# Optimization experiments

Hardware: AMD Instinct MI355X
Metric: run time of the kernel (lower is better)

The kernel has to match this reference:

```python
import math
import jax, jax.numpy as jnp
import numpy as np

DRAGON_ITERATIONS = 12
DRAGON_SMOOTHING = 0.1


def _dragon_patterns(iterations=DRAGON_ITERATIONS, smoothing=DRAGON_SMOOTHING):
    """Deterministic (non-learned) Dragon curve patterns, matching torch impl."""
    patterns = [np.array([0.5], dtype=np.float32)]
    kernel = np.ones(3, dtype=np.float32) / 3.0
    for _ in range(1, iterations):
        prev = patterns[-1]
        n = len(prev)
        newp = np.zeros(2 * n + 1, dtype=np.float32)
        newp[:n] = prev
        newp[n] = 0.5
        newp[n + 1:] = 1.0 - prev[::-1]
        if smoothing > 0:
            # conv1d with kernel_size=3, padding=1 (zero pad) == np.convolve 'same'
            newp = np.convolve(newp, kernel, mode='same').astype(np.float32)
        newp = (newp - newp.min()) / (newp.max() - newp.min() + 1e-8)
        patterns.append(newp.astype(np.float32))
    return patterns

_PATTERNS = _dragon_patterns()


def _interp_pattern(seq_len):
    """Linearly interpolate selected dragon pattern to seq_len (static shapes)."""
    it = min(int(math.log2(seq_len)), DRAGON_ITERATIONS - 1)
    pattern = _PATTERNS[it]
    if len(pattern) == seq_len:
        w = pattern.copy()
    else:
        x_old = np.linspace(0.0, 1.0, len(pattern), dtype=np.float64)
        x_new = np.linspace(0.0, 1.0, seq_len, dtype=np.float64)
        w = np.interp(x_new, x_old, pattern.astype(np.float64)).astype(np.float32)
    return it, jnp.asarray(w)


def setup_inputs() -> dict:
    key = jax.random.key(0)
    ks = jax.random.split(key, 8)
    B, S, D = 8, 2048, 512
    query = jax.random.normal(ks[0], (B, S, D), dtype=jnp.float32)
    k = jax.random.normal(ks[1], (B, S, D), dtype=jnp.float32)
    value = jax.random.normal(ks[2], (B, S, D), dtype=jnp.float32)
    pattern_scale = jnp.ones((DRAGON_ITERATIONS,), dtype=jnp.float32)
    pattern_bias = jnp.zeros((DRAGON_ITERATIONS,), dtype=jnp.float32)
    w1 = jax.random.normal(ks[3], (DRAGON_ITERATIONS, 64), dtype=jnp.float32) * (1.0 / math.sqrt(DRAGON_ITERATIONS))
    b1 = jnp.zeros((64,), dtype=jnp.float32)
    w2 = jax.random.normal(ks[4], (64, 1), dtype=jnp.float32) * (1.0 / 8.0)
    b2 = jnp.zeros((1,), dtype=jnp.float32)
    return {"query": query, "key": k, "value": value,
            "pattern_scale": pattern_scale, "pattern_bias": pattern_bias,
            "w1": w1, "b1": b1, "w2": w2, "b2": b2}


def reference(query, key, value, pattern_scale, pattern_bias, w1, b1, w2, b2):
    B, S, D = key.shape
    it, base_w = _interp_pattern(S)
    # learned affine + softplus on dragon weights
    dragon_w = jax.nn.softplus(base_w * pattern_scale[it] + pattern_bias[it])  # [S]
    weighted_keys = key * dragon_w[None, :, None]                              # [B,S,D]
    scores = jnp.einsum('bqd,bkd->bqk', query, weighted_keys) / math.sqrt(D)   # [B,S,S]
    attn = jax.nn.softmax(scores, axis=-1)
    # blend factor from one-hot iteration features through tiny MLP
    feat = jax.nn.one_hot(it, DRAGON_ITERATIONS, dtype=query.dtype)            # [12]
    h = jax.nn.relu(feat @ w1 + b1)
    blend = jax.nn.sigmoid(h @ w2 + b2)                                        # [1]
    blend = blend[0]
    final_attn = blend * attn + (1.0 - blend) / S                              # uniform blend
    out = jnp.einsum('bqk,bkd->bqd', final_attn, value)                        # [B,S,D]
    # original does output.squeeze(1); S>1 so it's a no-op here
    return out
```

## Files before the change

kernel.cpp:

```cpp
#include <hip/hip_runtime.h>
#include <cstdint>

#define DEV __device__ __forceinline__

typedef float f32x4 __attribute__((ext_vector_type(4)));
typedef short s16x8 __attribute__((ext_vector_type(8)));

DEV unsigned short f2bf(float f){
    unsigned u = __builtin_bit_cast(unsigned, f);
    u = u + 0x7fffu + ((u >> 16) & 1u);
    return (unsigned short)(u >> 16);
}
DEV float bf2f(unsigned short h){
    unsigned u = ((unsigned)h) << 16;
    return __builtin_bit_cast(float, u);
}

typedef const void __attribute__((address_space(1)))* gcp;
typedef void __attribute__((address_space(3)))* lp;
DEV void gload_lds16(const void* g, void* l){
    __builtin_amdgcn_global_load_lds((gcp)g, (lp)l, 16, 0, 0);
}

DEV void bar(){ asm volatile("s_barrier" ::: "memory"); }
#define WAIT_VM(n) asm volatile("s_waitcnt vmcnt(" #n ")" ::: "memory")
#define LDSFENCE   asm volatile("s_waitcnt lgkmcnt(0)" ::: "memory")

__global__ __launch_bounds__(256) void k_stage1(
    const float* __restrict__ Q, const float* __restrict__ K,
    const float* __restrict__ V,
    const float* __restrict__ scale, const float* __restrict__ bias,
    const float* __restrict__ w1, const float* __restrict__ b1,
    const float* __restrict__ w2, const float* __restrict__ b2,
    float* __restrict__ dragon_w, float* __restrict__ blend_out,
    unsigned short* __restrict__ Qb, unsigned short* __restrict__ Kb,
    unsigned short* __restrict__ Vt, float* __restrict__ vmean_part)
{
    __shared__ float sh[8704];
    int tid = threadIdx.x;
    int bx  = blockIdx.x;

    if (bx == 0){
        float* A  = sh;
        float* Bb = sh + 4096;
        if (tid < 64){
            if (tid == 0) A[0] = 0.5f;
            LDSFENCE;
            int len = 1;
            const float third = 1.0f/3.0f;
            for (int it = 1; it < 12; ++it){
                int n = len, nl = 2*n + 1;
                for (int i = tid; i < nl; i += 64){
                    float v;
                    if (i < n)       v = A[i];
                    else if (i == n) v = 0.5f;
                    else             v = 1.0f - A[2*n - i];
                    Bb[i] = v;
                }
                LDSFENCE;
                float mn = 3.4e38f, mx = -3.4e38f;
                for (int i = tid; i < nl; i += 64){
                    float s = Bb[i]*third;
                    if (i > 0)    s += Bb[i-1]*third;
                    if (i < nl-1) s += Bb[i+1]*third;
                    A[i] = s;
                    mn = fminf(mn, s); mx = fmaxf(mx, s);
                }
                #pragma unroll
                for (int off = 32; off > 0; off >>= 1){
                    mn = fminf(mn, __shfl_xor(mn, off, 64));
                    mx = fmaxf(mx, __shfl_xor(mx, off, 64));
                }
                float lo = mn, den = mx - lo + 1e-8f;
                for (int i = tid; i < nl; i += 64) A[i] = (A[i] - lo) / den;
                LDSFENCE;
                len = nl;
            }
        }
        __syncthreads();
        float sc = scale[11], bi = bias[11];
        for (int i = tid; i < 2048; i += 256){
            float x = A[2*i]*sc + bi;
            dragon_w[i] = fmaxf(x, 0.f) + log1pf(__expf(-fabsf(x)));
        }
        if (tid < 64){
            float h = fmaxf(w1[11*64 + tid] + b1[tid], 0.f);
            float c = h * w2[tid];
            for (int off = 32; off > 0; off >>= 1) c += __shfl_xor(c, off, 64);
            if (tid == 0) blend_out[0] = 1.f/(1.f + __expf(-(c + b2[0])));
        }
        return;
    }

    if (bx <= 4096){
        const float* src = (bx <= 2048) ? Q : K;
        unsigned short* dst = (bx <= 2048) ? Qb : Kb;
        int bi = (bx <= 2048) ? (bx-1) : (bx-2049);
        const long long total4 = (long long)8*2048*512/4;
        long long stride = 2048LL*256;
        for (long long i = (long long)bi*256 + tid; i < total4; i += stride){
            long long base = i*4;
            const float4 q = *(const float4*)(src + base);
            ushort4 qo;
            qo.x = f2bf(q.x); qo.y = f2bf(q.y); qo.z = f2bf(q.z); qo.w = f2bf(q.w);
            *(ushort4*)(dst + base) = qo;
        }
        return;
    }

    int t = bx - 4097;
    int stile = t & 31, dtile = (t >> 5) & 7, b = t >> 8;
    int s0 = stile*64, d0 = dtile*64;
    float (*tile)[67] = (float(*)[67])sh;
    float* red = sh + 4288;
    int c4 = tid & 15, rr = tid >> 4;
    const float* src = V + ((long long)b*2048 + s0)*512 + d0;
    #pragma unroll
    for (int p = 0; p < 4; ++p){
        int row = p*16 + rr;
        const float4 v = *(const float4*)(src + (long long)row*512 + c4*4);
        tile[row][c4*4+0] = v.x; tile[row][c4*4+1] = v.y;
        tile[row][c4*4+2] = v.z; tile[row][c4*4+3] = v.w;
    }
    __syncthreads();
    unsigned short* dst = Vt + ((long long)b*512 + d0)*2048 + s0;
    #pragma unroll
    for (int p = 0; p < 4; ++p){
        int d = p*16 + rr;
        ushort4 o;
        o.x = f2bf(tile[c4*4+0][d]);
        o.y = f2bf(tile[c4*4+1][d]);
        o.z = f2bf(tile[c4*4+2][d]);
        o.w = f2bf(tile[c4*4+3][d]);
        *(ushort4*)(dst + (long long)d*2048 + c4*4) = o;
    }
    int dcol = tid & 63, sp = tid >> 6;
    float s = 0.f;
    #pragma unroll
    for (int ii = 0; ii < 16; ++ii) s += tile[sp*16 + ii][dcol];
    red[sp*64 + dcol] = s;
    __syncthreads();
    if (sp == 0){
        float tot = red[dcol] + red[64+dcol] + red[128+dcol] + red[192+dcol];
        vmean_part[stile*4096 + b*512 + d0 + dcol] = tot * (1.0f/2048.0f);
    }
}

#define SCALE_QK 0.04419417382415922f

__global__ __launch_bounds__(256) void k_gemm_qk(
    const unsigned short* __restrict__ Qb, const unsigned short* __restrict__ Kb,
    const float* __restrict__ dragon_w,
    unsigned short* __restrict__ Sp, float* __restrict__ lpart)
{
    __shared__ unsigned short A0[128*64], B0[128*64];
    __shared__ unsigned short A1[128*64], B1[128*64];
    int tid = threadIdx.x;
    int lane = tid & 63, wave = tid >> 6;
    int wm = wave >> 1, wn = wave & 1;
    int ln = lane & 15, q4 = lane >> 4;
    int sx = ln & 7;
    int lid = (blockIdx.x & 7)*256 + (blockIdx.x >> 3);
    int kb = lid & 15, qb = (lid >> 4) & 15, b = lid >> 8;
    int q0 = qb*128, k0 = kb*128;
    const unsigned short* Abase = Qb + ((long long)b*2048 + q0)*512;
    const unsigned short* Bbase = Kb + ((long long)b*2048 + k0)*512;

    f32x4 acc[4][4];
    #pragma unroll
    for (int i = 0; i < 4; ++i)
        #pragma unroll
        for (int j = 0; j < 4; ++j) acc[i][j] = (f32x4)0.0f;

    int cc = lane & 7;
    int rg = lane >> 3;

    auto STAGE = [&](unsigned short* dA, unsigned short* dB, int kt){
        #pragma unroll
        for (int c = 0; c < 4; ++c){
            int chunk = wave*4 + c;
            int row = chunk*8 + rg;
            int gc  = cc ^ (row & 7);
            gload_lds16(Abase + (long long)row*512 + kt*64 + gc*8, dA + chunk*512);
            gload_lds16(Bbase + (long long)row*512 + kt*64 + gc*8, dB + chunk*512);
        }
    };
    auto COMPUTE = [&](const unsigned short* At, const unsigned short* Bt){
        #pragma unroll
        for (int ks = 0; ks < 2; ++ks){
            s16x8 af[4], bfr[4];
            int cs = ((ks*4 + q4) ^ sx) * 8;
            #pragma unroll
            for (int i = 0; i < 4; ++i)
                af[i] = *(const s16x8*)&At[(wm*64 + i*16 + ln)*64 + cs];
            #pragma unroll
            for (int j = 0; j < 4; ++j)
                bfr[j] = *(const s16x8*)&Bt[(wn*64 + j*16 + ln)*64 + cs];
            __builtin_amdgcn_s_setprio(1);
            #pragma unroll
            for (int i = 0; i < 4; ++i)
                #pragma unroll
                for (int j = 0; j < 4; ++j)
                    acc[i][j] = __builtin_amdgcn_mfma_f32_16x16x32_bf16(af[i], bfr[j], acc[i][j], 0, 0, 0);
            __builtin_amdgcn_s_setprio(0);
        }
    };

    STAGE(A0, B0, 0);
    STAGE(A1, B1, 1);
    WAIT_VM(8); bar();
    #pragma unroll
    for (int t = 0; t < 8; ++t){
        if (t & 1) COMPUTE(A1, B1); else COMPUTE(A0, B0);
        bar();
        int tn = (t + 2) & 7;
        if (t & 1) STAGE(A1, B1, tn); else STAGE(A0, B0, tn);
        WAIT_VM(8);
        bar();
    }
    WAIT_VM(0); bar();

    float wj[4];
    #pragma unroll
    for (int j = 0; j < 4; ++j)
        wj[j] = dragon_w[k0 + wn*64 + j*16 + ln] * SCALE_QK;

    float* lred = (float*)A0;
    unsigned short* outp = Sp + (long long)b*2048*2048;
    #pragma unroll
    for (int i = 0; i < 4; ++i){
        float rs[4] = {0.f, 0.f, 0.f, 0.f};
        #pragma unroll
        for (int j = 0; j < 4; ++j){
            #pragma unroll
            for (int r = 0; r < 4; ++r){
                int q = q0 + wm*64 + i*16 + q4*4 + r;
                int k = k0 + wn*64 + j*16 + ln;
                float v = __expf(acc[i][j][r] * wj[j]);
                unsigned short h = f2bf(v);
                outp[(long long)q*2048 + k] = h;
                rs[r] += bf2f(h);
            }
        }
        #pragma unroll
        for (int r = 0; r < 4; ++r){
            float v = rs[r];
            v += __shfl_xor(v, 1, 16);
            v += __shfl_xor(v, 2, 16);
            v += __shfl_xor(v, 4, 16);
            v += __shfl_xor(v, 8, 16);
            if (ln == 0) lred[(wm*64 + i*16 + q4*4 + r)*2 + wn] = v;
        }
    }
    __syncthreads();
    if (tid < 128)
        lpart[((long long)b*16 + kb)*2048 + q0 + tid] = lred[tid*2] + lred[tid*2+1];
}

__global__ __launch_bounds__(256) void k_gemm_pv(
    const unsigned short* __restrict__ Sp, const unsigned short* __restrict__ Vt,
    const float* __restrict__ lpart, const float* __restrict__ vmean_part,
    const float* __restrict__ blendp, float* __restrict__ out)
{
    __shared__ unsigned short A0[128*64], B0[128*64];
    __shared__ unsigned short A1[128*64], B1[128*64];
    int tid = threadIdx.x;
    int lane = tid & 63, wave = tid >> 6;
    int wm = wave >> 1, wn = wave & 1;
    int ln = lane & 15, q4 = lane >> 4;
    int sx = ln & 7;
    int lid = (blockIdx.x & 7)*64 + (blockIdx.x >> 3);
    int db = lid & 3, qb = (lid >> 2) & 15, b = lid >> 6;
    int q0 = qb*128, d0 = db*128;
    const unsigned short* Abase = Sp + (long long)b*2048*2048 + (long long)q0*2048;
    const unsigned short* Bbase = Vt + ((long long)b*512 + d0)*2048;

    f32x4 acc[4][4];
    #pragma unroll
    for (int i = 0; i < 4; ++i)
        #pragma unroll
        for (int j = 0; j < 4; ++j) acc[i][j] = (f32x4)0.0f;

    int cc = lane & 7;
    int rg = lane >> 3;

    auto STAGE = [&](unsigned short* dA, unsigned short* dB, int kt){
        #pragma unroll
        for (int c = 0; c < 4; ++c){
            int chunk = wave*4 + c;
            int row = chunk*8 + rg;
            int gc  = cc ^ (row & 7);
            gload_lds16(Abase + (long long)row*2048 + kt*64 + gc*8, dA + chunk*512);
            gload_lds16(Bbase + (long long)row*2048 + kt*64 + gc*8, dB + chunk*512);
        }
    };
    auto COMPUTE = [&](const unsigned short* At, const unsigned short* Bt){
        #pragma unroll
        for (int ks = 0; ks < 2; ++ks){
            s16x8 af[4], bfr[4];
            int cs = ((ks*4 + q4) ^ sx) * 8;
            #pragma unroll
            for (int i = 0; i < 4; ++i)
                af[i] = *(const s16x8*)&At[(wm*64 + i*16 + ln)*64 + cs];
            #pragma unroll
            for (int j = 0; j < 4; ++j)
                bfr[j] = *(const s16x8*)&Bt[(wn*64 + j*16 + ln)*64 + cs];
            __builtin_amdgcn_s_setprio(1);
            #pragma unroll
            for (int i = 0; i < 4; ++i)
                #pragma unroll
                for (int j = 0; j < 4; ++j)
                    acc[i][j] = __builtin_amdgcn_mfma_f32_16x16x32_bf16(af[i], bfr[j], acc[i][j], 0, 0, 0);
            __builtin_amdgcn_s_setprio(0);
        }
    };

    STAGE(A0, B0, 0);
    STAGE(A1, B1, 1);
    WAIT_VM(8); bar();
    for (int t = 0; t < 32; ++t){
        if (t & 1) COMPUTE(A1, B1); else COMPUTE(A0, B0);
        bar();
        int tn = (t + 2) & 31;
        if (t & 1) STAGE(A1, B1, tn); else STAGE(A0, B0, tn);
        WAIT_VM(8);
        bar();
    }
    WAIT_VM(0); bar();

    float* l_sh  = (float*)A0;
    float* vm_sh = (float*)B0;
    if (tid < 128){
        float s = 0.f;
        #pragma unroll
        for (int kb = 0; kb < 16; ++kb)
            s += lpart[((long long)b*16 + kb)*2048 + q0 + tid];
        l_sh[tid] = 1.0f / s;
    } else {
        int d = tid - 128;
        float s = 0.f;
        #pragma unroll
        for (int st = 0; st < 32; ++st)
            s += vmean_part[st*4096 + b*512 + d0 + d];
        vm_sh[d] = s;
    }
    __syncthreads();

    float blend = blendp[0];
    float ib = 1.0f - blend;
    float* obase = out + ((long long)b*2048 + q0)*512 + d0;
    float vm[4];
    #pragma unroll
    for (int j = 0; j < 4; ++j) vm[j] = vm_sh[wn*64 + j*16 + ln];
    #pragma unroll
    for (int i = 0; i < 4; ++i){
        #pragma unroll
        for (int r = 0; r < 4; ++r){
            int ql = wm*64 + i*16 + q4*4 + r;
            float linv = l_sh[ql];
            #pragma unroll
            for (int j = 0; j < 4; ++j){
                int dl = wn*64 + j*16 + ln;
                obase[(long long)ql*512 + dl] = blend*acc[i][j][r]*linv + ib*vm[j];
            }
        }
    }
}

extern "C" void kernel_launch(void* const* d_in, const int* in_sizes, int n_in,
                              void* d_out, int out_size, void* d_ws, size_t ws_size,
                              hipStream_t stream)
{
    (void)in_sizes; (void)n_in; (void)out_size; (void)ws_size;
    const float* Q  = (const float*)d_in[0];
    const float* K  = (const float*)d_in[1];
    const float* V  = (const float*)d_in[2];
    const float* ps = (const float*)d_in[3];
    const float* pb = (const float*)d_in[4];
    const float* w1 = (const float*)d_in[5];
    const float* b1 = (const float*)d_in[6];
    const float* w2 = (const float*)d_in[7];
    const float* b2 = (const float*)d_in[8];
    float* out = (float*)d_out;

    char* ws = (char*)d_ws;
    float* dragon_w        = (float*)(ws);
    float* blend           = (float*)(ws + 8192);
    float* vmean_part      = (float*)(ws + 32768);
    size_t off = 32768 + (size_t)512*1024;
    unsigned short* Qb     = (unsigned short*)(ws + off);
    unsigned short* Kb     = (unsigned short*)(ws + off + (size_t)16*1024*1024);
    unsigned short* Vt     = (unsigned short*)(ws + off + (size_t)32*1024*1024);
    unsigned short* Sp     = (unsigned short*)(ws + off + (size_t)48*1024*1024);
    float* lpart           = (float*)(ws + off + (size_t)112*1024*1024);

    hipLaunchKernelGGL(k_stage1,  dim3(6145), dim3(256), 0, stream,
                       Q, K, V, ps, pb, w1, b1, w2, b2, dragon_w, blend,
                       Qb, Kb, Vt, vmean_part);
    hipLaunchKernelGGL(k_gemm_qk, dim3(2048), dim3(256), 0, stream,
                       Qb, Kb, dragon_w, Sp, lpart);
    hipLaunchKernelGGL(k_gemm_pv, dim3(512),  dim3(256), 0, stream,
                       Sp, Vt, lpart, vmean_part, blend, out);
}
```

Measured before the change: 243.6 us.

## Restructure PV GEMM into 256x128 tiles with triple-buffered half-step pipeline

The PV GEMM now uses 512-thread blocks covering 256 query rows by 128 head dims, with LDS buffers tripled and split into halves. Global-to-LDS loads for step t+2 are interleaved with MFMA work on the current step, with barriers and priority hints at each half. The QK kernel's main loop is rewritten as an unrolled stage/compute sequence using __syncthreads and without setprio. The aim is more operand reuse per block and better overlap of memory latency with MFMA work, at the cost of more LDS, fewer blocks and a more delicate synchronisation scheme.

```diff
diff --git a/kernel.cpp b/kernel.cpp
--- a/kernel.cpp
+++ b/kernel.cpp
@@ -196,29 +196,23 @@
             #pragma unroll
             for (int j = 0; j < 4; ++j)
                 bfr[j] = *(const s16x8*)&Bt[(wn*64 + j*16 + ln)*64 + cs];
-            __builtin_amdgcn_s_setprio(1);
             #pragma unroll
             for (int i = 0; i < 4; ++i)
                 #pragma unroll
                 for (int j = 0; j < 4; ++j)
                     acc[i][j] = __builtin_amdgcn_mfma_f32_16x16x32_bf16(af[i], bfr[j], acc[i][j], 0, 0, 0);
-            __builtin_amdgcn_s_setprio(0);
-        }
-    };
-
-    STAGE(A0, B0, 0);
-    STAGE(A1, B1, 1);
-    WAIT_VM(8); bar();
-    #pragma unroll
-    for (int t = 0; t < 8; ++t){
-        if (t & 1) COMPUTE(A1, B1); else COMPUTE(A0, B0);
-        bar();
-        int tn = (t + 2) & 7;
-        if (t & 1) STAGE(A1, B1, tn); else STAGE(A0, B0, tn);
-        WAIT_VM(8);
-        bar();
-    }
-    WAIT_VM(0); bar();
+        }
+    };
+
+    STAGE(A0, B0, 0); __syncthreads();
+    STAGE(A1, B1, 1); COMPUTE(A0, B0); __syncthreads();
+    STAGE(A0, B0, 2); COMPUTE(A1, B1); __syncthreads();
+    STAGE(A1, B1, 3); COMPUTE(A0, B0); __syncthreads();
+    STAGE(A0, B0, 4); COMPUTE(A1, B1); __syncthreads();
+    STAGE(A1, B1, 5); COMPUTE(A0, B0); __syncthreads();
+    STAGE(A0, B0, 6); COMPUTE(A1, B1); __syncthreads();
+    STAGE(A1, B1, 7); COMPUTE(A0, B0); __syncthreads();
+    COMPUTE(A1, B1); __syncthreads();
 
     float wj[4];
     #pragma unroll
@@ -257,23 +251,23 @@
         lpart[((long long)b*16 + kb)*2048 + q0 + tid] = lred[tid*2] + lred[tid*2+1];
 }
 
-__global__ __launch_bounds__(256) void k_gemm_pv(
+__global__ __launch_bounds__(512) void k_gemm_pv(
     const unsigned short* __restrict__ Sp, const unsigned short* __restrict__ Vt,
     const float* __restrict__ lpart, const float* __restrict__ vmean_part,
     const float* __restrict__ blendp, float* __restrict__ out)
 {
-    __shared__ unsigned short A0[128*64], B0[128*64];
-    __shared__ unsigned short A1[128*64], B1[128*64];
+    __shared__ unsigned short At[3][2][128*64];
+    __shared__ unsigned short Bt[3][2][64*64];
     int tid = threadIdx.x;
     int lane = tid & 63, wave = tid >> 6;
-    int wm = wave >> 1, wn = wave & 1;
+    int wm = wave & 3, wn = wave >> 2;
     int ln = lane & 15, q4 = lane >> 4;
-    int sx = ln & 7;
-    int lid = (blockIdx.x & 7)*64 + (blockIdx.x >> 3);
-    int db = lid & 3, qb = (lid >> 2) & 15, b = lid >> 6;
-    int q0 = qb*128, d0 = db*128;
-    const unsigned short* Abase = Sp + (long long)b*2048*2048 + (long long)q0*2048;
-    const unsigned short* Bbase = Vt + ((long long)b*512 + d0)*2048;
+    int cc = lane & 7, rg = lane >> 3;
+    int lid = (blockIdx.x & 7)*32 + (blockIdx.x >> 3);
+    int db = lid & 3, qb = (lid >> 2) & 7, b = lid >> 5;
+    int q0 = qb*256, d0 = db*128;
+    const unsigned short* Ab = Sp + (long long)b*2048*2048 + (long long)q0*2048;
+    const unsigned short* Bb = Vt + ((long long)b*512 + d0)*2048;
 
     f32x4 acc[4][4];
     #pragma unroll
@@ -281,63 +275,82 @@
         #pragma unroll
         for (int j = 0; j < 4; ++j) acc[i][j] = (f32x4)0.0f;
 
-    int cc = lane & 7;
-    int rg = lane >> 3;
-
-    auto STAGE = [&](unsigned short* dA, unsigned short* dB, int kt){
-        #pragma unroll
-        for (int c = 0; c < 4; ++c){
-            int chunk = wave*4 + c;
-            int row = chunk*8 + rg;
-            int gc  = cc ^ (row & 7);
-            gload_lds16(Abase + (long long)row*2048 + kt*64 + gc*8, dA + chunk*512);
-            gload_lds16(Bbase + (long long)row*2048 + kt*64 + gc*8, dB + chunk*512);
-        }
-    };
-    auto COMPUTE = [&](const unsigned short* At, const unsigned short* Bt){
-        #pragma unroll
-        for (int ks = 0; ks < 2; ++ks){
-            s16x8 af[4], bfr[4];
-            int cs = ((ks*4 + q4) ^ sx) * 8;
-            #pragma unroll
-            for (int i = 0; i < 4; ++i)
-                af[i] = *(const s16x8*)&At[(wm*64 + i*16 + ln)*64 + cs];
+    auto STAGE_A = [&](int ts, int h){
+        unsigned short* d = &At[ts % 3][h][0];
+        int tsrc = ts & 31;
+        #pragma unroll
+        for (int c2 = 0; c2 < 2; ++c2){
+            int c = wave*2 + c2;
+            int row = c*8 + rg;
+            gload_lds16(Ab + (long long)(h*128 + row)*2048 + tsrc*64 + (cc^rg)*8,
+                        d + c*512);
+        }
+    };
+    auto STAGE_B = [&](int ts, int g){
+        unsigned short* d = &Bt[ts % 3][g][0];
+        int tsrc = ts & 31;
+        int row = wave*8 + rg;
+        gload_lds16(Bb + (long long)(g*64 + row)*2048 + tsrc*64 + (cc^rg)*8,
+                    d + wave*512);
+    };
+    auto LDA = [&](int slot, int ks, s16x8* af){
+        const unsigned short* base = &At[slot][wm >> 1][0];
+        int cs = ((ks*4 + q4) ^ (ln & 7)) * 8;
+        #pragma unroll
+        for (int i = 0; i < 4; ++i)
+            af[i] = *(const s16x8*)&base[((wm&1)*64 + i*16 + ln)*64 + cs];
+    };
+    auto LDB = [&](int slot, int ks, s16x8* bf){
+        const unsigned short* base = &Bt[slot][wn][0];
+        int cs = ((ks*4 + q4) ^ (ln & 7)) * 8;
+        #pragma unroll
+        for (int j = 0; j < 4; ++j)
+            bf[j] = *(const s16x8*)&base[(j*16 + ln)*64 + cs];
+    };
+
+    STAGE_A(0,0); STAGE_A(0,1); STAGE_B(0,0); STAGE_B(0,1);
+    STAGE_A(1,0); STAGE_A(1,1); STAGE_B(1,0); STAGE_B(1,1);
+    WAIT_VM(6); bar();
+
+    for (int t = 0; t < 32; ++t){
+        int slot = t % 3;
+        s16x8 af[4], bf[4];
+        LDA(slot, 0, af); LDB(slot, 0, bf);
+        STAGE_A(t+2, 0); STAGE_B(t+2, 0);
+        bar(); LDSFENCE;
+        __builtin_amdgcn_s_setprio(1);
+        #pragma unroll
+        for (int i = 0; i < 4; ++i)
             #pragma unroll
             for (int j = 0; j < 4; ++j)
-                bfr[j] = *(const s16x8*)&Bt[(wn*64 + j*16 + ln)*64 + cs];
-            __builtin_amdgcn_s_setprio(1);
-            #pragma unroll
-            for (int i = 0; i < 4; ++i)
-                #pragma unroll
-                for (int j = 0; j < 4; ++j)
-                    acc[i][j] = __builtin_amdgcn_mfma_f32_16x16x32_bf16(af[i], bfr[j], acc[i][j], 0, 0, 0);
-            __builtin_amdgcn_s_setprio(0);
-        }
-    };
-
-    STAGE(A0, B0, 0);
-    STAGE(A1, B1, 1);
-    WAIT_VM(8); bar();
-    for (int t = 0; t < 32; ++t){
-        if (t & 1) COMPUTE(A1, B1); else COMPUTE(A0, B0);
+                acc[i][j] = __builtin_amdgcn_mfma_f32_16x16x32_bf16(af[i], bf[j], acc[i][j], 0, 0, 0);
+        __builtin_amdgcn_s_setprio(0);
         bar();
-        int tn = (t + 2) & 31;
-        if (t & 1) STAGE(A1, B1, tn); else STAGE(A0, B0, tn);
-        WAIT_VM(8);
+        LDA(slot, 1, af); LDB(slot, 1, bf);
+        STAGE_A(t+2, 1); STAGE_B(t+2, 1);
+        WAIT_VM(6);
+        bar(); LDSFENCE;
+        __builtin_amdgcn_s_setprio(1);
+        #pragma unroll
+        for (int i = 0; i < 4; ++i)
+            #pragma unroll
+            for (int j = 0; j < 4; ++j)
+                acc[i][j] = __builtin_amdgcn_mfma_f32_16x16x32_bf16(af[i], bf[j], acc[i][j], 0, 0, 0);
+        __builtin_amdgcn_s_setprio(0);
         bar();
     }
     WAIT_VM(0); bar();
 
-    float* l_sh  = (float*)A0;
-    float* vm_sh = (float*)B0;
-    if (tid < 128){
+    float* l_sh  = (float*)&At[0][0][0];
+    float* vm_sh = (float*)&Bt[0][0][0];
+    if (tid < 256){
         float s = 0.f;
         #pragma unroll
         for (int kb = 0; kb < 16; ++kb)
             s += lpart[((long long)b*16 + kb)*2048 + q0 + tid];
         l_sh[tid] = 1.0f / s;
-    } else {
-        int d = tid - 128;
+    } else if (tid < 384){
+        int d = tid - 256;
         float s = 0.f;
         #pragma unroll
         for (int st = 0; st < 32; ++st)
@@ -399,6 +412,6 @@
                        Qb, Kb, Vt, vmean_part);
     hipLaunchKernelGGL(k_gemm_qk, dim3(2048), dim3(256), 0, stream,
                        Qb, Kb, dragon_w, Sp, lpart);
-    hipLaunchKernelGGL(k_gemm_pv, dim3(512),  dim3(256), 0, stream,
+    hipLaunchKernelGGL(k_gemm_pv, dim3(256),  dim3(512), 0, stream,
                        Sp, Vt, lpart, vmean_part, blend, out);
 }
```

After: 251.3 us. 3.1% more time.
